# Performance work log

Measured on AMD Instinct MI355X. Metric: run time of the kernel, lower is better.

## Reference

```python
import jax, jax.numpy as jnp
import numpy as np
import itertools

R = 32  # voxel resolution
B, CIN, COUT, N, SD = 4, 32, 64, 32768, 256


def group_norm(x, gamma, beta, eps=1e-5):
    # torch GroupNorm with g = min(8, C) adjusted for divisibility
    C = x.shape[1]
    g = min(8, C)
    while g > 1 and C % g:
        g -= 1
    b = x.shape[0]
    xs = x.reshape(b, g, C // g, -1)
    mu = xs.mean(axis=(2, 3), keepdims=True)
    var = xs.var(axis=(2, 3), keepdims=True)
    xn = ((xs - mu) / jnp.sqrt(var + eps)).reshape(x.shape)
    shp = (1, C) + (1,) * (x.ndim - 2)
    return xn * gamma.reshape(shp) + beta.reshape(shp)


def conv1x1(w, x):  # w: (O, C), x: (B, C, N)
    return jnp.einsum('oc,bcn->bon', w, x)


def conv3d(x, w):  # x: (B,C,D,H,W), w: (O,I,3,3,3), padding 1
    return jax.lax.conv_general_dilated(x, w, (1, 1, 1), 'SAME',
                                        dimension_numbers=('NCDHW', 'OIDHW', 'NCDHW'))


def normalize_coords(coords):  # (B,N,3) -> [0, R-1]
    vmin = coords.min(axis=1, keepdims=True)
    vmax = coords.max(axis=1, keepdims=True)
    return (coords - vmin) / jnp.maximum(vmax - vmin, 1e-8) * (R - 1)


def voxelize(feats_bcn, norm):  # average voxelization via scatter-add
    b, C, n = feats_bcn.shape
    idx = jnp.clip(jnp.round(norm), 0, R - 1).astype(jnp.int32)  # (B,N,3)
    flat = (idx[..., 0] * R + idx[..., 1]) * R + idx[..., 2]  # (B,N)
    f_bnc = feats_bcn.transpose(0, 2, 1)
    seg = jax.vmap(lambda f, i: jax.ops.segment_sum(f, i, num_segments=R ** 3))(f_bnc, flat)
    cnt = jax.vmap(lambda i: jax.ops.segment_sum(jnp.ones((n,), feats_bcn.dtype), i, num_segments=R ** 3))(flat)
    vox = seg / jnp.maximum(cnt, 1.0)[..., None]  # (B, R^3, C)
    return vox.transpose(0, 2, 1).reshape(b, C, R, R, R)


def devoxelize(vox, norm):  # trilinear interpolation gather
    b, C = vox.shape[:2]
    n = norm.shape[1]
    f = jnp.clip(norm, 0.0, R - 1)
    x0 = jnp.floor(f)
    fr = f - x0
    x0i = x0.astype(jnp.int32)
    idxs, wts = [], []
    for d in itertools.product((0, 1), repeat=3):
        dv = jnp.array(d, jnp.int32)
        ci = jnp.minimum(x0i + dv, R - 1)  # (B,N,3)
        w = jnp.prod(jnp.where(jnp.array(d, bool), fr, 1.0 - fr), axis=-1)  # (B,N)
        idxs.append((ci[..., 0] * R + ci[..., 1]) * R + ci[..., 2])
        wts.append(w)
    idx8 = jnp.stack(idxs, axis=-1)  # (B,N,8)
    w8 = jnp.stack(wts, axis=-1)  # (B,N,8)
    vf = vox.reshape(b, C, R ** 3)
    g = jnp.take_along_axis(vf, idx8.reshape(b, 1, n * 8), axis=2).reshape(b, C, n, 8)
    return jnp.einsum('bcnk,bnk->bcn', g, w8)


def setup_inputs() -> dict:
    key = jax.random.key(0)
    ks = jax.random.split(key, 12)
    s = 0.05
    return {
        'feats': jax.random.normal(ks[0], (B, CIN, N), jnp.float32),
        'coords': jax.random.uniform(ks[1], (B, N, 3), jnp.float32),
        'style': jax.random.normal(ks[2], (B, SD), jnp.float32),
        'w_pin': jax.random.normal(ks[3], (COUT, CIN), jnp.float32) * s,
        'g_pin': jnp.ones((COUT,), jnp.float32), 'b_pin': jnp.zeros((COUT,), jnp.float32),
        'w_v1': jax.random.normal(ks[4], (COUT, COUT, 3, 3, 3), jnp.float32) * s,
        'g_v1': jnp.ones((COUT,), jnp.float32), 'b_v1': jnp.zeros((COUT,), jnp.float32),
        'w_v2': jax.random.normal(ks[5], (COUT, COUT, 3, 3, 3), jnp.float32) * s,
        'g_v2': jnp.ones((COUT,), jnp.float32), 'b_v2': jnp.zeros((COUT,), jnp.float32),
        'w_fuse': jax.random.normal(ks[6], (COUT, COUT), jnp.float32) * s,
        'g_f': jnp.ones((COUT,), jnp.float32), 'b_f': jnp.zeros((COUT,), jnp.float32),
        'w_skip': jax.random.normal(ks[7], (COUT, CIN), jnp.float32) * s,
        'w_as': jax.random.normal(ks[8], (COUT, SD), jnp.float32) * s,
        'b_as': jnp.zeros((COUT,), jnp.float32),
        'w_ab': jax.random.normal(ks[9], (COUT, SD), jnp.float32) * s,
        'b_ab': jnp.zeros((COUT,), jnp.float32),
    }


def reference(feats, coords, style, w_pin, g_pin, b_pin, w_v1, g_v1, b_v1,
              w_v2, g_v2, b_v2, w_fuse, g_f, b_f, w_skip, w_as, b_as, w_ab, b_ab):
    silu = jax.nn.silu
    x_in = silu(group_norm(conv1x1(w_pin, feats), g_pin, b_pin))  # point_in
    norm = normalize_coords(coords)
    vox = voxelize(x_in, norm)
    vox = silu(group_norm(conv3d(vox, w_v1), g_v1, b_v1))
    vox = silu(group_norm(conv3d(vox, w_v2), g_v2, b_v2))
    devox = devoxelize(vox, norm)
    out = silu(group_norm(conv1x1(w_fuse, devox), g_f, b_f))  # fuse
    out = out + conv1x1(w_skip, feats)  # skip (c_in != c_out)
    s = (style @ w_as.T + b_as)[..., None]  # AdaIN scale (B, C, 1)
    bb = (style @ w_ab.T + b_ab)[..., None]
    return out * (1.0 + s) + bb
```

## Files before the change

### kernel.cpp

```cpp
#include <hip/hip_runtime.h>
#include <hip/hip_bf16.h>
#include <math.h>

#define RR   32
#define RB   4
#define CIN  32
#define CO   64
#define NP   32768
#define SD   256
#define NVOX (RR*RR*RR)
#define GRP  8
#define CPG  8
#define GN_CNT 262144.0f
#define PR   34
#define PSLICE (PR*PR*CO)
#define PROW   (PR*CO)
#define PVOL   ((size_t)PR*PR*PR*CO)

typedef __attribute__((ext_vector_type(8))) short short8;
typedef __attribute__((ext_vector_type(4))) float f32x4;
typedef __attribute__((ext_vector_type(16))) float f32x16;

__device__ inline float silu_f(float x){ return x / (1.f + __expf(-x)); }
__device__ inline float bf2f(ushort u){ uint v = ((uint)u)<<16; return *(float*)&v; }
__device__ inline ushort f2bf(float x){ __hip_bfloat16 h = __float2bfloat16(x); return *(ushort*)&h; }

__device__ inline void wpack_dev(const float* __restrict__ w, short* __restrict__ wp, int i){
    int l  = i & 63;
    int nt = (i>>6) & 1;
    int kc = (i>>7) & 3;
    int t  = i>>9;
    int oc = nt*32 + (l&31);
    int cib = kc*16 + (l>>5)*8;
    ushort out[8];
    #pragma unroll
    for (int j=0;j<8;j++) out[j] = f2bf(w[((oc*CO + cib + j))*27 + t]);
    *(uint4*)(wp + (size_t)i*8) = *(uint4*)out;
}

__global__ __launch_bounds__(256) void k_prep(const float* __restrict__ w_v1, const float* __restrict__ w_v2,
                      short* __restrict__ wp1, short* __restrict__ wp2,
                      const float* __restrict__ style, const float* __restrict__ w_as,
                      const float* __restrict__ b_as, const float* __restrict__ w_ab,
                      const float* __restrict__ b_ab, float* __restrict__ ada_s,
                      float* __restrict__ ada_b, float* __restrict__ stats,
                      const float* __restrict__ coords, float* __restrict__ vmm){
    __shared__ float smn[256][3], smx[256][3];
    int blk = blockIdx.x, t = threadIdx.x;
    if (blk < 54){
        int i = blk*256 + t;
        if (i < 27*4*2*64) wpack_dev(w_v1, wp1, i);
    } else if (blk < 108){
        int i = (blk-54)*256 + t;
        if (i < 27*4*2*64) wpack_dev(w_v2, wp2, i);
    } else if (blk == 108){
        stats[t] = 0.f;
        int b = t >> 6, o = t & 63;
        const float* st = style + b*SD;
        float accs = b_as[o], accb = b_ab[o];
        for (int k=0;k<SD;k++){ float sv = st[k]; accs += sv*w_as[o*SD+k]; accb += sv*w_ab[o*SD+k]; }
        ada_s[t]=accs; ada_b[t]=accb;
    } else {
        int b = blk - 109;
        float mn[3]={1e30f,1e30f,1e30f}, mx[3]={-1e30f,-1e30f,-1e30f};
        const float* cp = coords + (size_t)b*NP*3;
        for (int n=t;n<NP;n+=256){
            #pragma unroll
            for(int d=0;d<3;d++){ float v = cp[n*3+d]; mn[d]=fminf(mn[d],v); mx[d]=fmaxf(mx[d],v);}
        }
        #pragma unroll
        for(int d=0;d<3;d++){ smn[t][d]=mn[d]; smx[t][d]=mx[d]; }
        __syncthreads();
        for(int s=128;s>0;s>>=1){
            if(t<s){
                #pragma unroll
                for(int d=0;d<3;d++){
                    smn[t][d]=fminf(smn[t][d],smn[t+s][d]);
                    smx[t][d]=fmaxf(smx[t][d],smx[t+s][d]);
                }
            }
            __syncthreads();
        }
        if(t<3){ vmm[b*6+t]=smn[0][t]; vmm[b*6+3+t]=smx[0][t]; }
    }
}

__global__ __launch_bounds__(256) void k_count(const float* __restrict__ coords, const float* __restrict__ vmm,
                        int* __restrict__ pid, int* __restrict__ cnt, float4* __restrict__ nrm){
    int p = blockIdx.x*256 + threadIdx.x;
    int b = p >> 15, n = p & (NP-1);
    const float* cp = coords + (size_t)(b*NP + n)*3;
    int id[3];
    float nc[3];
    #pragma unroll
    for(int d=0;d<3;d++){
        float vmin = vmm[b*6+d], vmax = vmm[b*6+3+d];
        float nr = (cp[d]-vmin)/fmaxf(vmax-vmin,1e-8f)*(RR-1);
        nc[d] = fminf(fmaxf(nr,0.f),(float)(RR-1));
        int ii = (int)rintf(nr);
        id[d] = min(max(ii,0),RR-1);
    }
    int flat = (id[0]*RR + id[1])*RR + id[2];
    pid[p] = flat;
    nrm[p] = make_float4(nc[0],nc[1],nc[2],0.f);
    atomicAdd(&cnt[(b<<15)+flat], 1);
}

__global__ __launch_bounds__(1024) void k_scan(const int* __restrict__ cnt, int* __restrict__ offs,
                        int* __restrict__ cursor){
    int b = blockIdx.x, t = threadIdx.x;
    const int* c = cnt + (b<<15);
    int base = t*32;
    int pref[32];
    int s = 0;
    #pragma unroll
    for (int k4=0;k4<8;k4++){
        int4 q = *(const int4*)(c + base + k4*4);
        pref[k4*4+0]=s; s+=q.x;
        pref[k4*4+1]=s; s+=q.y;
        pref[k4*4+2]=s; s+=q.z;
        pref[k4*4+3]=s; s+=q.w;
    }
    int lane = t & 63, w = t >> 6;
    int inc = s;
    #pragma unroll
    for (int off=1; off<64; off<<=1){ int u = __shfl_up(inc, off); if (lane>=off) inc += u; }
    __shared__ int wsum[16];
    if (lane==63) wsum[w]=inc;
    __syncthreads();
    int wexcl=0;
    for (int i=0;i<w;i++) wexcl += wsum[i];
    int texcl = wexcl + inc - s;
    int* o = offs + (b<<15) + base;
    int* cu = cursor + (b<<15) + base;
    #pragma unroll
    for (int k=0;k<32;k++){ int v = texcl + pref[k]; o[k]=v; cu[k]=v; }
}

__global__ __launch_bounds__(256) void k_fill(const int* __restrict__ pid, int* __restrict__ cursor,
                       int* __restrict__ slotmap, const float4* __restrict__ nrm,
                       float4* __restrict__ nrm_s){
    int p = blockIdx.x*256 + threadIdx.x;
    int b = p >> 15;
    int v = pid[p];
    int slot = atomicAdd(&cursor[(b<<15)+v], 1);
    slotmap[p] = slot;
    nrm_s[(b<<15)+slot] = nrm[p];
}

__global__ __launch_bounds__(256) void k_pin(const float* __restrict__ feats, const float* __restrict__ w_pin,
                      const int* __restrict__ slotmap,
                      ushort* __restrict__ ybuf, float* __restrict__ stats){
    __shared__ float sred[GRP*2];
    int t = threadIdx.x;
    if (t<GRP*2) sred[t]=0.f;
    __syncthreads();
    int l = t & 63, wv = t >> 6;
    int lc = l & 31, h = l >> 5;
    int p = blockIdx.x*128 + wv*32 + lc;
    int b = p >> 15, n = p & (NP-1);
    short8 aw[2][2];
    #pragma unroll
    for (int nt=0;nt<2;nt++)
    #pragma unroll
    for (int kc=0;kc<2;kc++){
        ushort tmp[8];
        #pragma unroll
        for (int j=0;j<8;j++) tmp[j]=f2bf(w_pin[(nt*32+lc)*CIN + kc*16 + h*8 + j]);
        aw[nt][kc]=*(short8*)tmp;
    }
    const float* fp = feats + (size_t)b*CIN*NP + n;
    short8 bf[2];
    #pragma unroll
    for (int kc=0;kc<2;kc++){
        ushort tmp[8];
        #pragma unroll
        for (int j=0;j<8;j++) tmp[j]=f2bf(fp[(size_t)(kc*16+h*8+j)*NP]);
        bf[kc]=*(short8*)tmp;
    }
    f32x16 acc0={}, acc1={};
    #pragma unroll
    for (int kc=0;kc<2;kc++){
        acc0 = __builtin_amdgcn_mfma_f32_32x32x16_bf16(aw[0][kc], bf[kc], acc0, 0,0,0);
        acc1 = __builtin_amdgcn_mfma_f32_32x32x16_bf16(aw[1][kc], bf[kc], acc1, 0,0,0);
    }
    int slot = slotmap[p];
    ushort* yo = ybuf + ((size_t)(b<<15) + slot)*CO;
    float sg[8], qg[8];
    #pragma unroll
    for (int nt=0;nt<2;nt++){
        #pragma unroll
        for (int q=0;q<4;q++){
            ushort pk[4]; float s=0.f, qq=0.f;
            #pragma unroll
            for (int j=0;j<4;j++){
                float v = nt ? acc1[q*4+j] : acc0[q*4+j];
                pk[j]=f2bf(v); s+=v; qq+=v*v;
            }
            *(uint2*)(yo + nt*32 + q*8 + h*4) = *(uint2*)pk;
            sg[nt*4+q]=s; qg[nt*4+q]=qq;
        }
    }
    #pragma unroll
    for (int g=0;g<8;g++){
        float s=sg[g], q=qg[g];
        #pragma unroll
        for (int off=1; off<64; off<<=1){ s+=__shfl_xor(s,off); q+=__shfl_xor(q,off); }
        if (l==0){ atomicAdd(&sred[g*2],s); atomicAdd(&sred[g*2+1],q); }
    }
    __syncthreads();
    if (t<GRP){ atomicAdd(&stats[(b*GRP+t)*2], sred[t*2]); atomicAdd(&stats[(b*GRP+t)*2+1], sred[t*2+1]); }
}

__global__ __launch_bounds__(256) void k_gather_pad(const ushort* __restrict__ ybuf, const int* __restrict__ offs,
                             const float* __restrict__ stats,
                             const float* __restrict__ gamma, const float* __restrict__ beta,
                             ushort* __restrict__ P){
    int i = blockIdx.x*256 + threadIdx.x;
    int c8 = i & 7;
    int vox = (i>>3) & (NVOX-1);
    int b = i >> 18;
    float s = stats[(b*GRP+c8)*2], qq = stats[(b*GRP+c8)*2+1];
    float m = s/GN_CNT;
    float inv = rsqrtf(qq/GN_CNT - m*m + 1e-5f);
    float ga[8], be[8];
    #pragma unroll
    for (int k=0;k<8;k++){ ga[k]=gamma[c8*8+k]*inv; be[k]=beta[c8*8+k]-m*ga[k]; }
    int o0 = offs[(b<<15)+vox];
    int o1 = (vox==NVOX-1) ? NP : offs[(b<<15)+vox+1];
    float acc[8];
    #pragma unroll
    for (int k=0;k<8;k++) acc[k]=0.f;
    for (int j=o0; j<o1; j++){
        uint4 raw = *(const uint4*)(ybuf + ((size_t)((b<<15)+j))*CO + c8*8);
        ushort* us = (ushort*)&raw;
        #pragma unroll
        for (int k=0;k<8;k++){
            float x = bf2f(us[k])*ga[k] + be[k];
            acc[k] += silu_f(x);
        }
    }
    float rc = (o1>o0) ? 1.f/(float)(o1-o0) : 0.f;
    ushort out[8];
    #pragma unroll
    for (int k=0;k<8;k++) out[k]=f2bf(acc[k]*rc);
    int u = vox>>10, v = (vox>>5)&31, w = vox&31;
    size_t pd = ((size_t)b*PVOL) + (size_t)(u+1)*PSLICE + (v+1)*PROW + (w+1)*CO + c8*8;
    *(uint4*)(P + pd) = *(uint4*)out;
}

__global__ __launch_bounds__(256, 2) void k_conv_mfma(const __hip_bfloat16* __restrict__ P,
                        const short* __restrict__ wpack,
                        __hip_bfloat16* __restrict__ outv, float* __restrict__ stats){
    __shared__ __align__(16) char lds[10*4352 + 24576];
    char* wlds = lds + 10*4352;
    int t = threadIdx.x;
    int blk = blockIdx.x;
    int vt = blk & 3;
    int u  = (blk >> 2) & 31;
    int b  = blk >> 7;
    int v0 = vt*8;

    const ushort* Pp = (const ushort*)P;
    int l  = t & 63;
    int wv = t >> 6;
    int lr = l & 31;
    int lh = l >> 5;

    f32x16 acc00 = {}, acc01 = {}, acc10 = {}, acc11 = {};

    for (int dz = 0; dz < 3; dz++){
        for (int i = t; i < 2720; i += 256){
            int r = i / 272;
            int chunk = i - r*272;
            size_t src = (size_t)b*PVOL + (size_t)(u+dz)*PSLICE + (size_t)(v0+r)*PROW + (size_t)chunk*8;
            uint4 val = *(const uint4*)(Pp + src);
            int vx = chunk >> 3;
            int colb = (chunk & 7) << 4;
            *(uint4*)(lds + r*4352 + vx*128 + (colb ^ ((vx&7)<<4))) = val;
        }
        for (int dy = 0; dy < 3; dy++){
            const uint4* wsrc = (const uint4*)(wpack + (size_t)(dz*9 + dy*3)*4096);
            uint4* wdst = (uint4*)wlds;
            #pragma unroll
            for (int i=0;i<6;i++) wdst[t + i*256] = wsrc[t + i*256];
            __syncthreads();
            #pragma unroll
            for (int dx = 0; dx < 3; dx++){
                int vx = lr + dx;
                int sw = (vx & 7) << 4;
                int ra = (2*wv + dy)*4352 + vx*128;
                int wb = dx*8192 + l*16;
                #pragma unroll
                for (int kc = 0; kc < 4; kc++){
                    short8 bw0 = *(const short8*)(wlds + wb + kc*2048);
                    short8 bw1 = *(const short8*)(wlds + wb + kc*2048 + 1024);
                    int col = (kc*32 + lh*16) ^ sw;
                    short8 av0 = *(const short8*)(lds + ra + col);
                    short8 av1 = *(const short8*)(lds + ra + 4352 + col);
                    acc00 = __builtin_amdgcn_mfma_f32_32x32x16_bf16(av0, bw0, acc00, 0, 0, 0);
                    acc01 = __builtin_amdgcn_mfma_f32_32x32x16_bf16(av0, bw1, acc01, 0, 0, 0);
                    acc10 = __builtin_amdgcn_mfma_f32_32x32x16_bf16(av1, bw0, acc10, 0, 0, 0);
                    acc11 = __builtin_amdgcn_mfma_f32_32x32x16_bf16(av1, bw1, acc11, 0, 0, 0);
                }
            }
            __syncthreads();
        }
    }

    ushort* ob = (ushort*)outv;
    float s0 = 0.f, q0 = 0.f, s1 = 0.f, q1 = 0.f;
    size_t vrow0 = ((size_t)(b*32 + u)*32 + v0 + 2*wv);
    #pragma unroll
    for (int reg = 0; reg < 16; reg++){
        int x = (reg&3) + 8*(reg>>2) + 4*lh;
        float a, c;
        a = acc00[reg]; c = acc01[reg];
        s0 += a; q0 += a*a; s1 += c; q1 += c*c;
        ob[(vrow0*32 + x)*CO + lr]      = f2bf(a);
        ob[(vrow0*32 + x)*CO + 32 + lr] = f2bf(c);
        a = acc10[reg]; c = acc11[reg];
        s0 += a; q0 += a*a; s1 += c; q1 += c*c;
        ob[((vrow0+1)*32 + x)*CO + lr]      = f2bf(a);
        ob[((vrow0+1)*32 + x)*CO + 32 + lr] = f2bf(c);
    }
    #pragma unroll
    for (int off : {1,2,4,32}){
        s0 += __shfl_xor(s0, off); q0 += __shfl_xor(q0, off);
        s1 += __shfl_xor(s1, off); q1 += __shfl_xor(q1, off);
    }
    if (lh==0 && (lr&7)==0){
        int g0 = lr>>3;
        atomicAdd(&stats[(b*GRP+g0)*2],     s0);
        atomicAdd(&stats[(b*GRP+g0)*2+1],   q0);
        atomicAdd(&stats[(b*GRP+4+g0)*2],   s1);
        atomicAdd(&stats[(b*GRP+4+g0)*2+1], q1);
    }
}

__global__ __launch_bounds__(256) void k_gnfin_cast(const __hip_bfloat16* __restrict__ raw, const float* __restrict__ stats,
                        const float* __restrict__ gamma, const float* __restrict__ beta,
                        __hip_bfloat16* __restrict__ P){
    int i = blockIdx.x*256 + threadIdx.x;
    int c8 = i & 7;
    int vox = (i>>3) & (NVOX-1);
    int b = i >> 18;
    float s = stats[(b*GRP+c8)*2], qq = stats[(b*GRP+c8)*2+1];
    float m = s/GN_CNT;
    float inv = rsqrtf(qq/GN_CNT - m*m + 1e-5f);
    uint4 rv = *(const uint4*)((const ushort*)raw + ((size_t)i)*8);
    ushort* us = (ushort*)&rv;
    ushort out[8];
    #pragma unroll
    for (int j=0;j<8;j++){
        int c = c8*8+j;
        float x = (bf2f(us[j]) - m)*inv*gamma[c] + beta[c];
        out[j] = f2bf(silu_f(x));
    }
    int u = vox>>10, v = (vox>>5)&31, w = vox&31;
    size_t pd = ((size_t)b*PVOL) + (size_t)(u+1)*PSLICE + (v+1)*PROW + (w+1)*CO + c8*8;
    *(uint4*)((ushort*)P + pd) = *(uint4*)out;
}

__global__ __launch_bounds__(256) void k_devox_fuse(const __hip_bfloat16* __restrict__ vox_,
                             const float4* __restrict__ nrm_s, const float* __restrict__ wf,
                             const float* __restrict__ st2, const float* __restrict__ g_v2,
                             const float* __restrict__ b_v2,
                             ushort* __restrict__ obuf, float* __restrict__ stats){
    __shared__ float sred[GRP*2];
    int t = threadIdx.x;
    if (t<GRP*2) sred[t]=0.f;
    __syncthreads();
    int l = t & 63, wv = t >> 6;
    int lc = l & 31, h = l >> 5;
    int j_ = blockIdx.x*128 + wv*32 + lc;
    int b = j_ >> 15;
    short8 aw[2][4];
    #pragma unroll
    for (int nt=0;nt<2;nt++)
    #pragma unroll
    for (int kc=0;kc<4;kc++){
        ushort tmp[8];
        #pragma unroll
        for (int j=0;j<8;j++) tmp[j]=f2bf(wf[(nt*32+lc)*CO + kc*16 + h*8 + j]);
        aw[nt][kc]=*(short8*)tmp;
    }
    float ga[4][8], be[4][8];
    #pragma unroll
    for (int kc=0;kc<4;kc++){
        int g = kc*2 + h;
        float s = st2[(b*GRP+g)*2], qq = st2[(b*GRP+g)*2+1];
        float m = s/GN_CNT;
        float inv = rsqrtf(qq/GN_CNT - m*m + 1e-5f);
        #pragma unroll
        for (int j=0;j<8;j++){
            int c = kc*16 + h*8 + j;
            ga[kc][j] = g_v2[c]*inv;
            be[kc][j] = b_v2[c] - m*ga[kc][j];
        }
    }
    float4 nr4 = nrm_s[j_];
    float f3[3] = {nr4.x, nr4.y, nr4.z};
    float fr[3]; int x0[3];
    #pragma unroll
    for(int d=0;d<3;d++){
        float fl = floorf(f3[d]);
        x0[d]=(int)fl; fr[d]=f3[d]-fl;
    }
    float dev[4][8] = {};
    const ushort* vb = (const ushort*)vox_ + (size_t)b*NVOX*CO;
    #pragma unroll
    for (int k=0;k<8;k++){
        int d0=(k>>2)&1, d1=(k>>1)&1, d2=k&1;
        int i0=min(x0[0]+d0,RR-1), i1=min(x0[1]+d1,RR-1), i2=min(x0[2]+d2,RR-1);
        float w = (d0?fr[0]:1.f-fr[0])*(d1?fr[1]:1.f-fr[1])*(d2?fr[2]:1.f-fr[2]);
        const ushort* vp = vb + (size_t)((i0*RR+i1)*RR+i2)*CO + h*8;
        #pragma unroll
        for (int kc=0;kc<4;kc++){
            uint4 rv = *(const uint4*)(vp + kc*16);
            ushort* us = (ushort*)&rv;
            #pragma unroll
            for (int j=0;j<8;j++){
                float x = bf2f(us[j])*ga[kc][j] + be[kc][j];
                dev[kc][j] += w * silu_f(x);
            }
        }
    }
    short8 bf[4];
    #pragma unroll
    for (int kc=0;kc<4;kc++){
        ushort tmp[8];
        #pragma unroll
        for (int j=0;j<8;j++) tmp[j]=f2bf(dev[kc][j]);
        bf[kc]=*(short8*)tmp;
    }
    f32x16 acc0={}, acc1={};
    #pragma unroll
    for (int kc=0;kc<4;kc++){
        acc0 = __builtin_amdgcn_mfma_f32_32x32x16_bf16(aw[0][kc], bf[kc], acc0, 0,0,0);
        acc1 = __builtin_amdgcn_mfma_f32_32x32x16_bf16(aw[1][kc], bf[kc], acc1, 0,0,0);
    }
    ushort* op = obuf + (size_t)j_*CO;
    float sg[8], qg[8];
    #pragma unroll
    for (int nt=0;nt<2;nt++){
        #pragma unroll
        for (int q=0;q<4;q++){
            ushort pk[4]; float s=0.f, qq=0.f;
            #pragma unroll
            for (int j=0;j<4;j++){
                float v = nt ? acc1[q*4+j] : acc0[q*4+j];
                pk[j]=f2bf(v); s+=v; qq+=v*v;
            }
            *(uint2*)(op + nt*32 + q*8 + h*4) = *(uint2*)pk;
            sg[nt*4+q]=s; qg[nt*4+q]=qq;
        }
    }
    #pragma unroll
    for (int g=0;g<8;g++){
        float s=sg[g], q=qg[g];
        #pragma unroll
        for (int off=1; off<64; off<<=1){ s+=__shfl_xor(s,off); q+=__shfl_xor(q,off); }
        if (l==0){ atomicAdd(&sred[g*2],s); atomicAdd(&sred[g*2+1],q); }
    }
    __syncthreads();
    if (t<GRP){ atomicAdd(&stats[(b*GRP+t)*2], sred[t*2]); atomicAdd(&stats[(b*GRP+t)*2+1], sred[t*2+1]); }
}

__global__ __launch_bounds__(256) void k_final(const ushort* __restrict__ obuf, const int* __restrict__ slotmap,
                        const float* __restrict__ stats,
                        const float* __restrict__ gamma, const float* __restrict__ beta,
                        const float* __restrict__ feats, const float* __restrict__ wskip,
                        const float* __restrict__ ada_s, const float* __restrict__ ada_b,
                        float* __restrict__ out){
    int t = threadIdx.x;
    int l = t & 63, wv = t >> 6;
    int lc = l & 31, h = l >> 5;
    int p = blockIdx.x*128 + wv*32 + lc;
    int b = p >> 15, n = p & (NP-1);
    short8 aw[2][2];
    #pragma unroll
    for (int nt=0;nt<2;nt++)
    #pragma unroll
    for (int kc=0;kc<2;kc++){
        ushort tmp[8];
        #pragma unroll
        for (int j=0;j<8;j++) tmp[j]=f2bf(wskip[(nt*32+lc)*CIN + kc*16 + h*8 + j]);
        aw[nt][kc]=*(short8*)tmp;
    }
    const float* fp = feats + (size_t)b*CIN*NP + n;
    short8 bf[2];
    #pragma unroll
    for (int kc=0;kc<2;kc++){
        ushort tmp[8];
        #pragma unroll
        for (int j=0;j<8;j++) tmp[j]=f2bf(fp[(size_t)(kc*16+h*8+j)*NP]);
        bf[kc]=*(short8*)tmp;
    }
    f32x16 acc0={}, acc1={};
    #pragma unroll
    for (int kc=0;kc<2;kc++){
        acc0 = __builtin_amdgcn_mfma_f32_32x32x16_bf16(aw[0][kc], bf[kc], acc0, 0,0,0);
        acc1 = __builtin_amdgcn_mfma_f32_32x32x16_bf16(aw[1][kc], bf[kc], acc1, 0,0,0);
    }
    float mean[GRP], inv[GRP];
    #pragma unroll
    for (int g=0; g<GRP; g++){
        float s=stats[(b*GRP+g)*2], q=stats[(b*GRP+g)*2+1];
        float m=s/GN_CNT;
        mean[g]=m; inv[g]=rsqrtf(q/GN_CNT - m*m + 1e-5f);
    }
    int slot = slotmap[p];
    const ushort* ip = obuf + ((size_t)(b<<15) + slot)*CO;
    float* op = out + (size_t)b*CO*NP + n;
    #pragma unroll
    for (int nt=0;nt<2;nt++){
        #pragma unroll
        for (int q=0;q<4;q++){
            uint2 raw = *(const uint2*)(ip + nt*32 + q*8 + h*4);
            ushort* us = (ushort*)&raw;
            int g = nt*4 + q;
            #pragma unroll
            for (int j=0;j<4;j++){
                int oc = nt*32 + q*8 + h*4 + j;
                float u = (bf2f(us[j]) - mean[g])*inv[g]*gamma[oc] + beta[oc];
                u = silu_f(u);
                float sk = nt ? acc1[q*4+j] : acc0[q*4+j];
                float s = ada_s[b*CO+oc], bb = ada_b[b*CO+oc];
                op[(size_t)oc*NP] = (u+sk)*(1.f+s)+bb;
            }
        }
    }
}

extern "C" void kernel_launch(void* const* d_in, const int* in_sizes, int n_in,
                              void* d_out, int out_size, void* d_ws, size_t ws_size,
                              hipStream_t stream){
    const float* feats =(const float*)d_in[0];
    const float* coords=(const float*)d_in[1];
    const float* style =(const float*)d_in[2];
    const float* w_pin =(const float*)d_in[3];
    const float* g_pin =(const float*)d_in[4];
    const float* b_pin =(const float*)d_in[5];
    const float* w_v1  =(const float*)d_in[6];
    const float* g_v1  =(const float*)d_in[7];
    const float* b_v1  =(const float*)d_in[8];
    const float* w_v2  =(const float*)d_in[9];
    const float* g_v2  =(const float*)d_in[10];
    const float* b_v2  =(const float*)d_in[11];
    const float* w_fuse=(const float*)d_in[12];
    const float* g_f   =(const float*)d_in[13];
    const float* b_f   =(const float*)d_in[14];
    const float* w_skip=(const float*)d_in[15];
    const float* w_as  =(const float*)d_in[16];
    const float* b_as  =(const float*)d_in[17];
    const float* w_ab  =(const float*)d_in[18];
    const float* b_ab  =(const float*)d_in[19];
    float* out=(float*)d_out;
    char* ws =(char*)d_ws;

    ushort* ybuf  = (ushort*)ws;
    ushort* Pvol  = (ushort*)(ws + 16777216);
    ushort* raw   = (ushort*)(ws + 16777216 + 20123648);
    char*   small = ws + 16777216 + 20123648 + 16777216;
    float* stats  = (float*)small;
    float* vmm    = stats + 256;
    float* ada_s  = vmm + 24;
    float* ada_b  = ada_s + RB*CO;
    short* wp1    = (short*)(ada_b + RB*CO);
    short* wp2    = wp1 + 27*4*2*64*8;
    int*   pid    = (int*)(wp2 + 27*4*2*64*8);
    int*   cnt    = pid + RB*NP;
    int*   offs   = cnt + RB*NVOX;
    int*   cursor = offs + RB*NVOX;
    int*   slotmap= cursor + RB*NVOX;
    float4* nrm4  = (float4*)(slotmap + RB*NP);
    float4* nrm_s = nrm4 + RB*NP;
    ushort* obuf  = ybuf;

    float* st0 = stats;
    float* st1 = stats + 64;
    float* st2 = stats + 128;
    float* st3 = stats + 192;

    hipMemsetAsync(cnt, 0, (size_t)RB*NVOX*sizeof(int), stream);
    hipMemsetAsync(Pvol, 0, (size_t)RB*PVOL*sizeof(ushort), stream);

    k_prep<<<113,256,0,stream>>>(w_v1,w_v2,wp1,wp2,style,w_as,b_as,w_ab,b_ab,
                                 ada_s,ada_b,stats,coords,vmm);
    k_count<<<RB*NP/256,256,0,stream>>>(coords,vmm,pid,cnt,nrm4);
    k_scan<<<RB,1024,0,stream>>>(cnt,offs,cursor);
    k_fill<<<RB*NP/256,256,0,stream>>>(pid,cursor,slotmap,nrm4,nrm_s);
    k_pin<<<RB*NP/128,256,0,stream>>>(feats,w_pin,slotmap,ybuf,st0);
    k_gather_pad<<<RB*NVOX*8/256,256,0,stream>>>(ybuf,offs,st0,g_pin,b_pin,Pvol);

    k_conv_mfma<<<RB*RR*4,256,0,stream>>>((const __hip_bfloat16*)Pvol, wp1, (__hip_bfloat16*)raw, st1);
    k_gnfin_cast<<<RB*NVOX*8/256,256,0,stream>>>((const __hip_bfloat16*)raw, st1, g_v1, b_v1, (__hip_bfloat16*)Pvol);
    k_conv_mfma<<<RB*RR*4,256,0,stream>>>((const __hip_bfloat16*)Pvol, wp2, (__hip_bfloat16*)raw, st2);

    k_devox_fuse<<<RB*NP/128,256,0,stream>>>((const __hip_bfloat16*)raw, nrm_s, w_fuse,
                                             st2, g_v2, b_v2, obuf, st3);
    k_final<<<RB*NP/128,256,0,stream>>>(obuf, slotmap, st3, g_f, b_f, feats, w_skip, ada_s, ada_b, out);
}
```

Measured before the change: 385.7 us.

## Fuse point binning into one LDS sort kernel and zero the padding halo inline

```diff
diff --git a/kernel.cpp b/kernel.cpp
--- a/kernel.cpp
+++ b/kernel.cpp
@@ -16,6 +16,7 @@
 #define PSLICE (PR*PR*CO)
 #define PROW   (PR*CO)
 #define PVOL   ((size_t)PR*PR*PR*CO)
+#define CPB    314432
 
 typedef __attribute__((ext_vector_type(8))) short short8;
 typedef __attribute__((ext_vector_type(4))) float f32x4;
@@ -43,9 +44,7 @@
                       const float* __restrict__ style, const float* __restrict__ w_as,
                       const float* __restrict__ b_as, const float* __restrict__ w_ab,
                       const float* __restrict__ b_ab, float* __restrict__ ada_s,
-                      float* __restrict__ ada_b, float* __restrict__ stats,
-                      const float* __restrict__ coords, float* __restrict__ vmm){
-    __shared__ float smn[256][3], smx[256][3];
+                      float* __restrict__ ada_b, float* __restrict__ stats){
     int blk = blockIdx.x, t = threadIdx.x;
     if (blk < 54){
         int i = blk*256 + t;
@@ -53,99 +52,97 @@
     } else if (blk < 108){
         int i = (blk-54)*256 + t;
         if (i < 27*4*2*64) wpack_dev(w_v2, wp2, i);
-    } else if (blk == 108){
+    } else {
         stats[t] = 0.f;
         int b = t >> 6, o = t & 63;
         const float* st = style + b*SD;
         float accs = b_as[o], accb = b_ab[o];
         for (int k=0;k<SD;k++){ float sv = st[k]; accs += sv*w_as[o*SD+k]; accb += sv*w_ab[o*SD+k]; }
         ada_s[t]=accs; ada_b[t]=accb;
-    } else {
-        int b = blk - 109;
-        float mn[3]={1e30f,1e30f,1e30f}, mx[3]={-1e30f,-1e30f,-1e30f};
-        const float* cp = coords + (size_t)b*NP*3;
-        for (int n=t;n<NP;n+=256){
-            #pragma unroll
-            for(int d=0;d<3;d++){ float v = cp[n*3+d]; mn[d]=fminf(mn[d],v); mx[d]=fmaxf(mx[d],v);}
-        }
-        #pragma unroll
-        for(int d=0;d<3;d++){ smn[t][d]=mn[d]; smx[t][d]=mx[d]; }
-        __syncthreads();
-        for(int s=128;s>0;s>>=1){
-            if(t<s){
-                #pragma unroll
-                for(int d=0;d<3;d++){
-                    smn[t][d]=fminf(smn[t][d],smn[t+s][d]);
-                    smx[t][d]=fmaxf(smx[t][d],smx[t+s][d]);
-                }
-            }
-            __syncthreads();
-        }
-        if(t<3){ vmm[b*6+t]=smn[0][t]; vmm[b*6+3+t]=smx[0][t]; }
-    }
-}
-
-__global__ __launch_bounds__(256) void k_count(const float* __restrict__ coords, const float* __restrict__ vmm,
-                        int* __restrict__ pid, int* __restrict__ cnt, float4* __restrict__ nrm){
-    int p = blockIdx.x*256 + threadIdx.x;
-    int b = p >> 15, n = p & (NP-1);
-    const float* cp = coords + (size_t)(b*NP + n)*3;
-    int id[3];
-    float nc[3];
-    #pragma unroll
-    for(int d=0;d<3;d++){
-        float vmin = vmm[b*6+d], vmax = vmm[b*6+3+d];
-        float nr = (cp[d]-vmin)/fmaxf(vmax-vmin,1e-8f)*(RR-1);
-        nc[d] = fminf(fmaxf(nr,0.f),(float)(RR-1));
-        int ii = (int)rintf(nr);
-        id[d] = min(max(ii,0),RR-1);
-    }
-    int flat = (id[0]*RR + id[1])*RR + id[2];
-    pid[p] = flat;
-    nrm[p] = make_float4(nc[0],nc[1],nc[2],0.f);
-    atomicAdd(&cnt[(b<<15)+flat], 1);
-}
-
-__global__ __launch_bounds__(1024) void k_scan(const int* __restrict__ cnt, int* __restrict__ offs,
-                        int* __restrict__ cursor){
+    }
+}
+
+__global__ __launch_bounds__(1024) void k_sort(const float* __restrict__ coords, int* __restrict__ offs,
+                        int* __restrict__ slotmap, float4* __restrict__ nrm_s){
+    __shared__ int lcnt[NVOX];
+    __shared__ float smm[16*6];
+    __shared__ int wsum[16];
     int b = blockIdx.x, t = threadIdx.x;
-    const int* c = cnt + (b<<15);
+    int lane = t & 63, w = t >> 6;
+    const float* cb = coords + (size_t)b*NP*3;
+    float mn[3]={1e30f,1e30f,1e30f}, mx[3]={-1e30f,-1e30f,-1e30f};
+    for (int k=0;k<32;k++){
+        int n = t + (k<<10);
+        #pragma unroll
+        for (int d=0;d<3;d++){ float v = cb[n*3+d]; mn[d]=fminf(mn[d],v); mx[d]=fmaxf(mx[d],v); }
+    }
+    #pragma unroll
+    for (int off=32; off>=1; off>>=1){
+        #pragma unroll
+        for (int d=0;d<3;d++){
+            mn[d] = fminf(mn[d], __shfl_xor(mn[d], off));
+            mx[d] = fmaxf(mx[d], __shfl_xor(mx[d], off));
+        }
+    }
+    if (lane==0){
+        #pragma unroll
+        for (int d=0;d<3;d++){ smm[w*6+d]=mn[d]; smm[w*6+3+d]=mx[d]; }
+    }
+    for (int k=t;k<NVOX;k+=1024) lcnt[k]=0;
+    __syncthreads();
+    float vmin[3], den[3];
+    #pragma unroll
+    for (int d=0;d<3;d++){
+        float a=1e30f, z=-1e30f;
+        for (int i=0;i<16;i++){ a=fminf(a,smm[i*6+d]); z=fmaxf(z,smm[i*6+3+d]); }
+        vmin[d]=a; den[d]=fmaxf(z-a,1e-8f);
+    }
+    int fl[32];
+    for (int k=0;k<32;k++){
+        int n = t + (k<<10);
+        int id[3];
+        #pragma unroll
+        for (int d=0;d<3;d++){
+            float nr = (cb[n*3+d]-vmin[d])/den[d]*(RR-1);
+            int ii = (int)rintf(nr);
+            id[d]=min(max(ii,0),RR-1);
+        }
+        fl[k] = (id[0]*RR+id[1])*RR+id[2];
+        atomicAdd(&lcnt[fl[k]],1);
+    }
+    __syncthreads();
     int base = t*32;
-    int pref[32];
-    int s = 0;
-    #pragma unroll
-    for (int k4=0;k4<8;k4++){
-        int4 q = *(const int4*)(c + base + k4*4);
-        pref[k4*4+0]=s; s+=q.x;
-        pref[k4*4+1]=s; s+=q.y;
-        pref[k4*4+2]=s; s+=q.z;
-        pref[k4*4+3]=s; s+=q.w;
-    }
-    int lane = t & 63, w = t >> 6;
+    int pref[32]; int s=0;
+    #pragma unroll
+    for (int k=0;k<32;k++){ pref[k]=s; s+=lcnt[base+k]; }
     int inc = s;
     #pragma unroll
     for (int off=1; off<64; off<<=1){ int u = __shfl_up(inc, off); if (lane>=off) inc += u; }
-    __shared__ int wsum[16];
     if (lane==63) wsum[w]=inc;
     __syncthreads();
     int wexcl=0;
     for (int i=0;i<w;i++) wexcl += wsum[i];
     int texcl = wexcl + inc - s;
-    int* o = offs + (b<<15) + base;
-    int* cu = cursor + (b<<15) + base;
-    #pragma unroll
-    for (int k=0;k<32;k++){ int v = texcl + pref[k]; o[k]=v; cu[k]=v; }
-}
-
-__global__ __launch_bounds__(256) void k_fill(const int* __restrict__ pid, int* __restrict__ cursor,
-                       int* __restrict__ slotmap, const float4* __restrict__ nrm,
-                       float4* __restrict__ nrm_s){
-    int p = blockIdx.x*256 + threadIdx.x;
-    int b = p >> 15;
-    int v = pid[p];
-    int slot = atomicAdd(&cursor[(b<<15)+v], 1);
-    slotmap[p] = slot;
-    nrm_s[(b<<15)+slot] = nrm[p];
+    int* og = offs + (b<<15) + base;
+    #pragma unroll
+    for (int k=0;k<32;k++){
+        int v = texcl + pref[k];
+        og[k] = v;
+        lcnt[base+k] = v;
+    }
+    __syncthreads();
+    for (int k=0;k<32;k++){
+        int n = t + (k<<10);
+        int slot = atomicAdd(&lcnt[fl[k]],1);
+        slotmap[(b<<15)+n] = slot;
+        float nc[3];
+        #pragma unroll
+        for (int d=0;d<3;d++){
+            float nr = (cb[n*3+d]-vmin[d])/den[d]*(RR-1);
+            nc[d] = fminf(fmaxf(nr,0.f),(float)(RR-1));
+        }
+        nrm_s[(b<<15)+slot] = make_float4(nc[0],nc[1],nc[2],0.f);
+    }
 }
 
 __global__ __launch_bounds__(256) void k_pin(const float* __restrict__ feats, const float* __restrict__ w_pin,
@@ -217,9 +214,20 @@
                              const float* __restrict__ gamma, const float* __restrict__ beta,
                              ushort* __restrict__ P){
     int i = blockIdx.x*256 + threadIdx.x;
-    int c8 = i & 7;
-    int vox = (i>>3) & (NVOX-1);
-    int b = i >> 18;
+    int b = i / CPB;
+    int r = i - b*CPB;
+    ushort* dst = P + (size_t)b*PVOL + (size_t)r*8;
+    int pvox = r >> 3, c8 = r & 7;
+    int pu = pvox / (PR*PR);
+    int rem = pvox - pu*PR*PR;
+    int pv = rem / PR;
+    int pw = rem - pv*PR;
+    if (pu==0 || pu==PR-1 || pv==0 || pv==PR-1 || pw==0 || pw==PR-1){
+        uint4 z = {0,0,0,0};
+        *(uint4*)dst = z;
+        return;
+    }
+    int vox = ((pu-1)*RR + (pv-1))*RR + (pw-1);
     float s = stats[(b*GRP+c8)*2], qq = stats[(b*GRP+c8)*2+1];
     float m = s/GN_CNT;
     float inv = rsqrtf(qq/GN_CNT - m*m + 1e-5f);
@@ -244,9 +252,7 @@
     ushort out[8];
     #pragma unroll
     for (int k=0;k<8;k++) out[k]=f2bf(acc[k]*rc);
-    int u = vox>>10, v = (vox>>5)&31, w = vox&31;
-    size_t pd = ((size_t)b*PVOL) + (size_t)(u+1)*PSLICE + (v+1)*PROW + (w+1)*CO + c8*8;
-    *(uint4*)(P + pd) = *(uint4*)out;
+    *(uint4*)dst = *(uint4*)out;
 }
 
 __global__ __launch_bounds__(256, 2) void k_conv_mfma(const __hip_bfloat16* __restrict__ P,
@@ -564,18 +570,13 @@
     ushort* raw   = (ushort*)(ws + 16777216 + 20123648);
     char*   small = ws + 16777216 + 20123648 + 16777216;
     float* stats  = (float*)small;
-    float* vmm    = stats + 256;
-    float* ada_s  = vmm + 24;
+    float* ada_s  = stats + 256;
     float* ada_b  = ada_s + RB*CO;
     short* wp1    = (short*)(ada_b + RB*CO);
     short* wp2    = wp1 + 27*4*2*64*8;
-    int*   pid    = (int*)(wp2 + 27*4*2*64*8);
-    int*   cnt    = pid + RB*NP;
-    int*   offs   = cnt + RB*NVOX;
-    int*   cursor = offs + RB*NVOX;
-    int*   slotmap= cursor + RB*NVOX;
-    float4* nrm4  = (float4*)(slotmap + RB*NP);
-    float4* nrm_s = nrm4 + RB*NP;
+    int*   offs   = (int*)(wp2 + 27*4*2*64*8);
+    int*   slotmap= offs + RB*NVOX;
+    float4* nrm_s = (float4*)(slotmap + RB*NP);
     ushort* obuf  = ybuf;
 
     float* st0 = stats;
@@ -583,16 +584,11 @@
     float* st2 = stats + 128;
     float* st3 = stats + 192;
 
-    hipMemsetAsync(cnt, 0, (size_t)RB*NVOX*sizeof(int), stream);
-    hipMemsetAsync(Pvol, 0, (size_t)RB*PVOL*sizeof(ushort), stream);
-
-    k_prep<<<113,256,0,stream>>>(w_v1,w_v2,wp1,wp2,style,w_as,b_as,w_ab,b_ab,
-                                 ada_s,ada_b,stats,coords,vmm);
-    k_count<<<RB*NP/256,256,0,stream>>>(coords,vmm,pid,cnt,nrm4);
-    k_scan<<<RB,1024,0,stream>>>(cnt,offs,cursor);
-    k_fill<<<RB*NP/256,256,0,stream>>>(pid,cursor,slotmap,nrm4,nrm_s);
+    k_prep<<<109,256,0,stream>>>(w_v1,w_v2,wp1,wp2,style,w_as,b_as,w_ab,b_ab,
+                                 ada_s,ada_b,stats);
+    k_sort<<<RB,1024,0,stream>>>(coords,offs,slotmap,nrm_s);
     k_pin<<<RB*NP/128,256,0,stream>>>(feats,w_pin,slotmap,ybuf,st0);
-    k_gather_pad<<<RB*NVOX*8/256,256,0,stream>>>(ybuf,offs,st0,g_pin,b_pin,Pvol);
+    k_gather_pad<<<RB*CPB/256,256,0,stream>>>(ybuf,offs,st0,g_pin,b_pin,Pvol);
 
     k_conv_mfma<<<RB*RR*4,256,0,stream>>>((const __hip_bfloat16*)Pvol, wp1, (__hip_bfloat16*)raw, st1);
     k_gnfin_cast<<<RB*NVOX*8/256,256,0,stream>>>((const __hip_bfloat16*)raw, st1, g_v1, b_v1, (__hip_bfloat16*)Pvol);
```

Result: slower. 396.0 us (+2.7%).

## Fuse GroupNorm+SiLU into second conv input load and write padding in gather

Applied to the files above, without the earlier changes.

```diff
diff --git a/kernel.cpp b/kernel.cpp
--- a/kernel.cpp
+++ b/kernel.cpp
@@ -10,15 +10,14 @@
 #define SD   256
 #define NVOX (RR*RR*RR)
 #define GRP  8
-#define CPG  8
 #define GN_CNT 262144.0f
 #define PR   34
 #define PSLICE (PR*PR*CO)
 #define PROW   (PR*CO)
 #define PVOL   ((size_t)PR*PR*PR*CO)
+#define CPB    314432
 
 typedef __attribute__((ext_vector_type(8))) short short8;
-typedef __attribute__((ext_vector_type(4))) float f32x4;
 typedef __attribute__((ext_vector_type(16))) float f32x16;
 
 __device__ inline float silu_f(float x){ return x / (1.f + __expf(-x)); }
@@ -217,9 +216,20 @@
                              const float* __restrict__ gamma, const float* __restrict__ beta,
                              ushort* __restrict__ P){
     int i = blockIdx.x*256 + threadIdx.x;
-    int c8 = i & 7;
-    int vox = (i>>3) & (NVOX-1);
-    int b = i >> 18;
+    int b = i / CPB;
+    int r = i - b*CPB;
+    ushort* dst = P + (size_t)b*PVOL + (size_t)r*8;
+    int pvox = r >> 3, c8 = r & 7;
+    int pu = pvox / (PR*PR);
+    int rem = pvox - pu*PR*PR;
+    int pv = rem / PR;
+    int pw = rem - pv*PR;
+    if (pu==0 || pu==PR-1 || pv==0 || pv==PR-1 || pw==0 || pw==PR-1){
+        uint4 z = {0,0,0,0};
+        *(uint4*)dst = z;
+        return;
+    }
+    int vox = ((pu-1)*RR + (pv-1))*RR + (pw-1);
     float s = stats[(b*GRP+c8)*2], qq = stats[(b*GRP+c8)*2+1];
     float m = s/GN_CNT;
     float inv = rsqrtf(qq/GN_CNT - m*m + 1e-5f);
@@ -244,14 +254,15 @@
     ushort out[8];
     #pragma unroll
     for (int k=0;k<8;k++) out[k]=f2bf(acc[k]*rc);
-    int u = vox>>10, v = (vox>>5)&31, w = vox&31;
-    size_t pd = ((size_t)b*PVOL) + (size_t)(u+1)*PSLICE + (v+1)*PROW + (w+1)*CO + c8*8;
-    *(uint4*)(P + pd) = *(uint4*)out;
-}
-
-__global__ __launch_bounds__(256, 2) void k_conv_mfma(const __hip_bfloat16* __restrict__ P,
+    *(uint4*)dst = *(uint4*)out;
+}
+
+template<int FUSED>
+__global__ __launch_bounds__(256, 2) void k_conv(const ushort* __restrict__ in,
                         const short* __restrict__ wpack,
-                        __hip_bfloat16* __restrict__ outv, float* __restrict__ stats){
+                        const float* __restrict__ gst, const float* __restrict__ gg,
+                        const float* __restrict__ gb,
+                        ushort* __restrict__ outv, float* __restrict__ stats){
     __shared__ __align__(16) char lds[10*4352 + 24576];
     char* wlds = lds + 10*4352;
     int t = threadIdx.x;
@@ -261,7 +272,6 @@
     int b  = blk >> 7;
     int v0 = vt*8;
 
-    const ushort* Pp = (const ushort*)P;
     int l  = t & 63;
     int wv = t >> 6;
     int lr = l & 31;
@@ -273,11 +283,31 @@
         for (int i = t; i < 2720; i += 256){
             int r = i / 272;
             int chunk = i - r*272;
-            size_t src = (size_t)b*PVOL + (size_t)(u+dz)*PSLICE + (size_t)(v0+r)*PROW + (size_t)chunk*8;
-            uint4 val = *(const uint4*)(Pp + src);
             int vx = chunk >> 3;
-            int colb = (chunk & 7) << 4;
-            *(uint4*)(lds + r*4352 + vx*128 + (colb ^ ((vx&7)<<4))) = val;
+            int c8 = chunk & 7;
+            uint4 val;
+            if (FUSED){
+                int au = u + dz - 1, av = v0 + r - 1, ax = vx - 1;
+                val = make_uint4(0,0,0,0);
+                if ((unsigned)au < 32u && (unsigned)av < 32u && (unsigned)ax < 32u){
+                    uint4 rv = *(const uint4*)(in + ((size_t)(((b*32+au)*32+av)*32+ax))*CO + c8*8);
+                    float m = gst[(b*GRP+c8)*2]/GN_CNT;
+                    float iv = rsqrtf(gst[(b*GRP+c8)*2+1]/GN_CNT - m*m + 1e-5f);
+                    ushort* us = (ushort*)&rv;
+                    ushort o8[8];
+                    #pragma unroll
+                    for (int j=0;j<8;j++){
+                        int c = c8*8+j;
+                        float x = (bf2f(us[j]) - m)*iv*gg[c] + gb[c];
+                        o8[j] = f2bf(silu_f(x));
+                    }
+                    val = *(uint4*)o8;
+                }
+            } else {
+                size_t src = (size_t)b*PVOL + (size_t)(u+dz)*PSLICE + (size_t)(v0+r)*PROW + (size_t)chunk*8;
+                val = *(const uint4*)(in + src);
+            }
+            *(uint4*)(lds + r*4352 + vx*128 + ((c8<<4) ^ ((vx&7)<<4))) = val;
         }
         for (int dy = 0; dy < 3; dy++){
             const uint4* wsrc = (const uint4*)(wpack + (size_t)(dz*9 + dy*3)*4096);
@@ -308,7 +338,7 @@
         }
     }
 
-    ushort* ob = (ushort*)outv;
+    ushort* ob = outv;
     float s0 = 0.f, q0 = 0.f, s1 = 0.f, q1 = 0.f;
     size_t vrow0 = ((size_t)(b*32 + u)*32 + v0 + 2*wv);
     #pragma unroll
@@ -338,31 +368,7 @@
     }
 }
 
-__global__ __launch_bounds__(256) void k_gnfin_cast(const __hip_bfloat16* __restrict__ raw, const float* __restrict__ stats,
-                        const float* __restrict__ gamma, const float* __restrict__ beta,
-                        __hip_bfloat16* __restrict__ P){
-    int i = blockIdx.x*256 + threadIdx.x;
-    int c8 = i & 7;
-    int vox = (i>>3) & (NVOX-1);
-    int b = i >> 18;
-    float s = stats[(b*GRP+c8)*2], qq = stats[(b*GRP+c8)*2+1];
-    float m = s/GN_CNT;
-    float inv = rsqrtf(qq/GN_CNT - m*m + 1e-5f);
-    uint4 rv = *(const uint4*)((const ushort*)raw + ((size_t)i)*8);
-    ushort* us = (ushort*)&rv;
-    ushort out[8];
-    #pragma unroll
-    for (int j=0;j<8;j++){
-        int c = c8*8+j;
-        float x = (bf2f(us[j]) - m)*inv*gamma[c] + beta[c];
-        out[j] = f2bf(silu_f(x));
-    }
-    int u = vox>>10, v = (vox>>5)&31, w = vox&31;
-    size_t pd = ((size_t)b*PVOL) + (size_t)(u+1)*PSLICE + (v+1)*PROW + (w+1)*CO + c8*8;
-    *(uint4*)((ushort*)P + pd) = *(uint4*)out;
-}
-
-__global__ __launch_bounds__(256) void k_devox_fuse(const __hip_bfloat16* __restrict__ vox_,
+__global__ __launch_bounds__(256) void k_devox_fuse(const ushort* __restrict__ vox_,
                              const float4* __restrict__ nrm_s, const float* __restrict__ wf,
                              const float* __restrict__ st2, const float* __restrict__ g_v2,
                              const float* __restrict__ b_v2,
@@ -408,7 +414,7 @@
         x0[d]=(int)fl; fr[d]=f3[d]-fl;
     }
     float dev[4][8] = {};
-    const ushort* vb = (const ushort*)vox_ + (size_t)b*NVOX*CO;
+    const ushort* vb = vox_ + (size_t)b*NVOX*CO;
     #pragma unroll
     for (int k=0;k<8;k++){
         int d0=(k>>2)&1, d1=(k>>1)&1, d2=k&1;
@@ -576,6 +582,7 @@
     int*   slotmap= cursor + RB*NVOX;
     float4* nrm4  = (float4*)(slotmap + RB*NP);
     float4* nrm_s = nrm4 + RB*NP;
+    ushort* vox2  = Pvol;
     ushort* obuf  = ybuf;
 
     float* st0 = stats;
@@ -584,7 +591,6 @@
     float* st3 = stats + 192;
 
     hipMemsetAsync(cnt, 0, (size_t)RB*NVOX*sizeof(int), stream);
-    hipMemsetAsync(Pvol, 0, (size_t)RB*PVOL*sizeof(ushort), stream);
 
     k_prep<<<113,256,0,stream>>>(w_v1,w_v2,wp1,wp2,style,w_as,b_as,w_ab,b_ab,
                                  ada_s,ada_b,stats,coords,vmm);
@@ -592,13 +598,14 @@
     k_scan<<<RB,1024,0,stream>>>(cnt,offs,cursor);
     k_fill<<<RB*NP/256,256,0,stream>>>(pid,cursor,slotmap,nrm4,nrm_s);
     k_pin<<<RB*NP/128,256,0,stream>>>(feats,w_pin,slotmap,ybuf,st0);
-    k_gather_pad<<<RB*NVOX*8/256,256,0,stream>>>(ybuf,offs,st0,g_pin,b_pin,Pvol);
-
-    k_conv_mfma<<<RB*RR*4,256,0,stream>>>((const __hip_bfloat16*)Pvol, wp1, (__hip_bfloat16*)raw, st1);
-    k_gnfin_cast<<<RB*NVOX*8/256,256,0,stream>>>((const __hip_bfloat16*)raw, st1, g_v1, b_v1, (__hip_bfloat16*)Pvol);
-    k_conv_mfma<<<RB*RR*4,256,0,stream>>>((const __hip_bfloat16*)Pvol, wp2, (__hip_bfloat16*)raw, st2);
-
-    k_devox_fuse<<<RB*NP/128,256,0,stream>>>((const __hip_bfloat16*)raw, nrm_s, w_fuse,
+    k_gather_pad<<<RB*CPB/256,256,0,stream>>>(ybuf,offs,st0,g_pin,b_pin,Pvol);
+
+    k_conv<0><<<RB*RR*4,256,0,stream>>>(Pvol, wp1, nullptr, nullptr, nullptr,
+                                        raw, st1);
+    k_conv<1><<<RB*RR*4,256,0,stream>>>(raw, wp2, st1, g_v1, b_v1,
+                                        vox2, st2);
+
+    k_devox_fuse<<<RB*NP/128,256,0,stream>>>(vox2, nrm_s, w_fuse,
                                              st2, g_v2, b_v2, obuf, st3);
     k_final<<<RB*NP/128,256,0,stream>>>(obuf, slotmap, st3, g_f, b_f, feats, w_skip, ada_s, ada_b, out);
 }
```

New measurement: 375.8 us. 1.03x faster.
